# Kernel optimization log

Measured on AMD Instinct MI355X. Metric: run time of the kernel, lower is better.

Reference implementation:

```python
import jax, jax.numpy as jnp
import numpy as np

B, T, D, P, ALPHA, PR = 4, 4096, 1024, 512, 4, 64


def setup_inputs() -> dict:
    key = jax.random.key(0)
    ks = jax.random.split(key, 9)
    g = lambda k, shape, scale: jax.random.normal(k, shape, jnp.float32) * scale
    return {
        "x": jax.random.normal(ks[0], (B, T, D), jnp.float32),
        "W_toP": g(ks[1], (D, P), D ** -0.5),
        "W_U": g(ks[2], (D, P, ALPHA), D ** -0.5),
        "W_F": g(ks[3], (D, P), D ** -0.5),
        "W_V": g(ks[4], (P, ALPHA), 1.0),
        "W_lam": g(ks[5], (P, PR), P ** -0.5),
        "B_mat": g(ks[6], (P, PR), P ** -0.5),
        "C_mat": g(ks[7], (PR, P), PR ** -0.5),
        "W_fromP": g(ks[8], (P, D), P ** -0.5),
    }


def reference(x, W_toP, W_U, W_F, W_V, W_lam, B_mat, C_mat, W_fromP):
    # dense pre-path: (B,T,D)->(B,T,P)
    pre = jnp.einsum('btd,dp->btp', x, W_toP)
    # CeptaEmbedding dense pathway: multi-factor projection U, gates F, weighted Y
    U = jnp.einsum('btd,dpa->btpa', x, W_U)            # (B,T,P,alpha)
    Fg = jax.nn.sigmoid(jnp.einsum('btd,dp->btp', x, W_F))  # (B,T,P) in (0,1)
    Y = U * W_V                                        # (B,T,P,alpha)
    # CeptaRouting(reduce='sum'): sum over alpha factors, plus residual pre-path
    t = Y.sum(-1) + pre                                # (B,T,P)
    # CeptaSSMLowRank: input-dependent diagonal decay in rank-PR state space
    lam = jax.nn.sigmoid(jnp.einsum('btp,pr->btr', Fg, W_lam))  # (B,T,PR)
    u_in = jnp.einsum('btp,pr->btr', t, B_mat)                  # (B,T,PR)

    def step(s, inp):
        l, u = inp
        s = l * s + u
        return s, s

    s0 = jnp.zeros((x.shape[0], PR), x.dtype)
    _, s_seq = jax.lax.scan(step, s0, (lam.transpose(1, 0, 2), u_in.transpose(1, 0, 2)))
    s_seq = s_seq.transpose(1, 0, 2)                   # (B,T,PR)
    t_tilde = t + jnp.einsum('btr,rp->btp', s_seq, C_mat)
    h = jnp.einsum('btp,pd->btd', t_tilde, W_fromP)    # dropout p=0 -> identity
    return h
```

## Files before the change

kernel.cpp:

```cpp
#include <hip/hip_runtime.h>
#include <hip/hip_bf16.h>

#define Bb 4
#define Tt 4096
#define Dd 1024
#define Pp 512
#define PRr 64
#define Mm (Bb*Tt)
#define NCH 64
#define CL  64

typedef __bf16 bf16;
typedef __bf16 bf16x8 __attribute__((ext_vector_type(8)));
typedef __bf16 bf16x4 __attribute__((ext_vector_type(4)));
typedef float f32x4 __attribute__((ext_vector_type(4)));

#define GPTR(p) (const __attribute__((address_space(1))) void*)(p)
#define LPTR(p) (__attribute__((address_space(3))) void*)(p)

__device__ __forceinline__ float sigmoidf_(float x) {
    return 1.0f / (1.0f + __expf(-x));
}


__global__ void prep_w1(const float* __restrict__ W_toP, const float* __restrict__ W_U,
                        const float* __restrict__ W_V, const float* __restrict__ W_F,
                        bf16* __restrict__ W1t) {
    int idx = blockIdx.x * 256 + threadIdx.x;
    int n = idx >> 10, k = idx & 1023;
    float v;
    if (n < Pp) {
        int p = n;
        float4 u  = *(const float4*)(W_U + ((size_t)k * Pp + p) * 4);
        float4 wv = *(const float4*)(W_V + (size_t)p * 4);
        v = W_toP[(size_t)k * Pp + p] + u.x * wv.x + u.y * wv.y + u.z * wv.z + u.w * wv.w;
    } else {
        v = W_F[(size_t)k * Pp + (n - Pp)];
    }
    W1t[idx] = (bf16)v;
}

__global__ void prep_w3(const float* __restrict__ B_mat, const float* __restrict__ W_lam,
                        bf16* __restrict__ W3t) {
    int idx = blockIdx.x * 256 + threadIdx.x;
    int n = idx >> 10, k = idx & 1023;
    float v = 0.0f;
    if (n < PRr) { if (k < Pp) v = B_mat[(size_t)k * PRr + n]; }
    else         { if (k >= Pp) v = W_lam[(size_t)(k - Pp) * PRr + (n - PRr)]; }
    W3t[idx] = (bf16)v;
}

__global__ void prep_w2(const float* __restrict__ W_fromP, const float* __restrict__ C_mat,
                        bf16* __restrict__ W2t) {
    int n = blockIdx.x;
    int k = threadIdx.x;
    float v;
    if (k < Pp) {
        v = W_fromP[(size_t)k * Dd + n];
    } else {
        int r = k - Pp;
        float acc = 0.0f;
        #pragma unroll 8
        for (int p = 0; p < Pp; p++)
            acc = fmaf(C_mat[(size_t)r * Pp + p], W_fromP[(size_t)p * Dd + n], acc);
        v = acc;
    }
    W2t[(size_t)n * 576 + k] = (bf16)v;
}

__global__ void cast_x(const float* __restrict__ x, bf16* __restrict__ xb) {
    int i = blockIdx.x * 256 + threadIdx.x;
    float4 v = ((const float4*)x)[i];
    bf16x4 o;
    o[0] = (bf16)v.x; o[1] = (bf16)v.y; o[2] = (bf16)v.z; o[3] = (bf16)v.w;
    ((bf16x4*)xb)[i] = o;
}

__global__ void scan_phase1(const float* __restrict__ UL,
                            float* __restrict__ slocal, float* __restrict__ pprod,
                            float* __restrict__ carryS, float* __restrict__ carryP) {
    int b = blockIdx.y, c = blockIdx.x, r = threadIdx.x;
    const float* ulb = UL + ((size_t)b * Tt + (size_t)c * CL) * 128;
    float* sl = slocal + ((size_t)b * Tt + (size_t)c * CL) * PRr;
    float* pp = pprod  + ((size_t)b * Tt + (size_t)c * CL) * PRr;
    float s = 0.0f, p = 1.0f;
    for (int t0 = 0; t0 < CL; t0 += 16) {
        float uv[16], lv[16];
        #pragma unroll
        for (int i = 0; i < 16; i++) {
            uv[i] = ulb[(size_t)(t0 + i) * 128 + r];
            lv[i] = ulb[(size_t)(t0 + i) * 128 + 64 + r];
        }
        #pragma unroll
        for (int i = 0; i < 16; i++) {
            s = fmaf(lv[i], s, uv[i]);
            p *= lv[i];
            sl[(size_t)(t0 + i) * PRr + r] = s;
            pp[(size_t)(t0 + i) * PRr + r] = p;
        }
    }
    int ci = b * NCH + c;
    carryS[(size_t)ci * PRr + r] = s;
    carryP[(size_t)ci * PRr + r] = p;
}

__global__ void scan_phase2(const float* __restrict__ carryS, const float* __restrict__ carryP,
                            float* __restrict__ carryIn) {
    int b = blockIdx.x, r = threadIdx.x;
    float carry = 0.0f;
    for (int c0 = 0; c0 < NCH; c0 += 16) {
        float cs[16], cp[16];
        #pragma unroll
        for (int i = 0; i < 16; i++) {
            size_t idx = ((size_t)b * NCH + c0 + i) * PRr + r;
            cs[i] = carryS[idx];
            cp[i] = carryP[idx];
        }
        #pragma unroll
        for (int i = 0; i < 16; i++) {
            carryIn[((size_t)b * NCH + c0 + i) * PRr + r] = carry;
            carry = fmaf(cp[i], carry, cs[i]);
        }
    }
}

__global__ void scan_phase3(const float* __restrict__ slocal, const float* __restrict__ pprod,
                            const float* __restrict__ carryIn, bf16* __restrict__ sb) {
    int i = blockIdx.x * 256 + threadIdx.x;
    int r = i & (PRr - 1);
    int row = i >> 6;
    int b = row >> 12;
    int t = row & (Tt - 1);
    int c = t / CL;
    float carry = carryIn[((size_t)b * NCH + c) * PRr + r];
    sb[i] = (bf16)fmaf(pprod[i], carry, slocal[i]);
}

template <int EPI>
__global__ __launch_bounds__(512, 2) void gemm256(
    const bf16* __restrict__ A0, int lda0,
    const bf16* __restrict__ A1, int lda1, int ksplit,
    const bf16* __restrict__ Bt, int ldb, int K,
    void* __restrict__ Cout, int ldc, int sigcol) {

    __shared__ bf16 As[2][256 * 64];
    __shared__ bf16 Bs[2][256 * 64];

    const int tid  = threadIdx.x;
    const int lane = tid & 63;
    const int wid  = tid >> 6;
    const int wm   = wid >> 2;
    const int wn   = wid & 3;

    const int cpx = gridDim.x >> 3;
    const int bid = blockIdx.x;
    const int swz = (bid & 7) * cpx + (bid >> 3);
    const int mBase = (swz >> 2) * 256;
    const int nBase = (swz & 3) * 256;

    const int lr  = lane & 15;
    const int q16 = (lane >> 4) * 16;

    auto srcA = [&](int kt, const bf16*& src, int& lda, int& kc) {
        if (kt < ksplit) { src = A0; lda = lda0; kc = kt; }
        else             { src = A1; lda = lda1; kc = kt - ksplit; }
    };

    auto stage = [&](const bf16* src, int lda, int kc, int rowBase, bf16* lbuf, int rd) {
        int d = rd * 8192 + tid * 16;
        int L = d ^ (((d >> 7) & 7) << 4);
        int r = L >> 7;
        int c = (L & 127) >> 1;
        const bf16* g = src + (size_t)(rowBase + r) * lda + (kc + c);
        __builtin_amdgcn_global_load_lds(GPTR(g), LPTR((char*)lbuf + d), 16, 0, 0);
    };

    auto frag = [&](const bf16* lbuf, int r, int cb) -> bf16x8 {
        int flat = r * 128 + cb;
        int phys = flat ^ (((flat >> 7) & 7) << 4);
        return *(const bf16x8*)((const char*)lbuf + phys);
    };

    const int NT = K / 64;

    {
        const bf16* sa; int la, kc; srcA(0, sa, la, kc);
        stage(sa, la, kc, mBase, As[0], 0); stage(sa, la, kc, mBase, As[0], 1);
        stage(sa, la, kc, mBase, As[0], 2); stage(sa, la, kc, mBase, As[0], 3);
        stage(Bt, ldb, 0, nBase, Bs[0], 0); stage(Bt, ldb, 0, nBase, Bs[0], 1);
        stage(Bt, ldb, 0, nBase, Bs[0], 2); stage(Bt, ldb, 0, nBase, Bs[0], 3);
    }
    asm volatile("s_waitcnt vmcnt(0)" ::: "memory");
    __builtin_amdgcn_s_barrier();

    f32x4 acc[8][4] = {};
    bf16x8 aX[4], aY[4], b0[4], b1[4];

    #pragma unroll
    for (int i = 0; i < 4; ++i) aX[i] = frag(As[0], wm * 128 + i * 16 + lr, q16);
    #pragma unroll
    for (int i = 0; i < 4; ++i) b0[i] = frag(Bs[0], wn * 64 + i * 16 + lr, q16);

    for (int t = 0; t < NT; ++t) {
        bf16* Ac = As[t & 1];       bf16* Bc = Bs[t & 1];
        bf16* An = As[(t + 1) & 1]; bf16* Bn = Bs[(t + 1) & 1];
        const bool hn = (t + 1 < NT);

        if (hn) {
            const bf16* sa; int la, kc; srcA((t + 1) * 64, sa, la, kc);
            const int ktn = (t + 1) * 64;
            stage(sa, la, kc, mBase, An, 0); stage(sa, la, kc, mBase, An, 1);
            stage(sa, la, kc, mBase, An, 2); stage(sa, la, kc, mBase, An, 3);
            stage(Bt, ldb, ktn, nBase, Bn, 0); stage(Bt, ldb, ktn, nBase, Bn, 1);
            stage(Bt, ldb, ktn, nBase, Bn, 2); stage(Bt, ldb, ktn, nBase, Bn, 3);
        }

        #pragma unroll
        for (int i = 0; i < 4; ++i) aY[i] = frag(Ac, wm * 128 + (i + 4) * 16 + lr, q16);
        __builtin_amdgcn_s_setprio(1);
        #pragma unroll
        for (int m = 0; m < 4; ++m)
            #pragma unroll
            for (int n = 0; n < 4; ++n)
                acc[m][n] = __builtin_amdgcn_mfma_f32_16x16x32_bf16(aX[m], b0[n], acc[m][n], 0, 0, 0);
        __builtin_amdgcn_s_setprio(0);

        #pragma unroll
        for (int i = 0; i < 4; ++i) aX[i] = frag(Ac, wm * 128 + i * 16 + lr, 64 + q16);
        #pragma unroll
        for (int i = 0; i < 4; ++i) b1[i] = frag(Bc, wn * 64 + i * 16 + lr, 64 + q16);
        __builtin_amdgcn_s_setprio(1);
        #pragma unroll
        for (int m = 0; m < 4; ++m)
            #pragma unroll
            for (int n = 0; n < 4; ++n)
                acc[m + 4][n] = __builtin_amdgcn_mfma_f32_16x16x32_bf16(aY[m], b0[n], acc[m + 4][n], 0, 0, 0);
        __builtin_amdgcn_s_setprio(0);

        #pragma unroll
        for (int i = 0; i < 4; ++i) aY[i] = frag(Ac, wm * 128 + (i + 4) * 16 + lr, 64 + q16);
        __builtin_amdgcn_s_setprio(1);
        #pragma unroll
        for (int m = 0; m < 4; ++m)
            #pragma unroll
            for (int n = 0; n < 4; ++n)
                acc[m][n] = __builtin_amdgcn_mfma_f32_16x16x32_bf16(aX[m], b1[n], acc[m][n], 0, 0, 0);
        __builtin_amdgcn_s_setprio(0);

        __builtin_amdgcn_s_setprio(1);
        #pragma unroll
        for (int m = 0; m < 4; ++m)
            #pragma unroll
            for (int n = 0; n < 4; ++n)
                acc[m + 4][n] = __builtin_amdgcn_mfma_f32_16x16x32_bf16(aY[m], b1[n], acc[m + 4][n], 0, 0, 0);
        __builtin_amdgcn_s_setprio(0);

        if (hn) {
            asm volatile("s_waitcnt vmcnt(0)" ::: "memory");
            __builtin_amdgcn_s_barrier();
            #pragma unroll
            for (int i = 0; i < 4; ++i) aX[i] = frag(An, wm * 128 + i * 16 + lr, q16);
            #pragma unroll
            for (int i = 0; i < 4; ++i) b0[i] = frag(Bn, wn * 64 + i * 16 + lr, q16);
        }
    }

    const int lr4 = (lane >> 4) * 4;
    #pragma unroll
    for (int m = 0; m < 8; ++m) {
        #pragma unroll
        for (int n = 0; n < 4; ++n) {
            #pragma unroll
            for (int j = 0; j < 4; ++j) {
                int row = mBase + wm * 128 + m * 16 + lr4 + j;
                int col = nBase + wn * 64 + n * 16 + lr;
                float v = acc[m][n][j];
                if (EPI == 0) {
                    if (col >= sigcol) v = sigmoidf_(v);
                    ((bf16*)Cout)[(size_t)row * ldc + col] = (bf16)v;
                } else {
                    ((float*)Cout)[(size_t)row * ldc + col] = v;
                }
            }
        }
    }
}

template <int EPI>
__global__ __launch_bounds__(256) void gemm_bt(
    const bf16* __restrict__ A0, int lda0,
    const bf16* __restrict__ A1, int lda1, int ksplit,
    const bf16* __restrict__ Bt, int K,
    void* __restrict__ Cout, int ldc, int sigcol) {

    __shared__ bf16 As[128][32];
    __shared__ bf16 Bs[128][32];

    const int tid  = threadIdx.x;
    const int lane = tid & 63;
    const int wid  = tid >> 6;
    const int wr   = (wid >> 1) * 64;
    const int wc   = (wid & 1) * 64;
    const int mBase = blockIdx.x * 128;
    const int nBase = blockIdx.y * 128;

    f32x4 acc[4][4] = {};

    const int lr = lane & 15;
    const int lk = (lane >> 4) * 8;

    for (int kt = 0; kt < K; kt += 32) {
        const bf16* Asrc; int lda_; int kcol;
        if (kt < ksplit) { Asrc = A0; lda_ = lda0; kcol = kt; }
        else             { Asrc = A1; lda_ = lda1; kcol = kt - ksplit; }

        __syncthreads();
        #pragma unroll
        for (int i = 0; i < 2; i++) {
            int c = tid + i * 256;
            int row = c >> 2, k8 = (c & 3) * 8;
            const bf16* g = Asrc + (size_t)(mBase + row) * lda_ + (kcol + k8);
            __builtin_amdgcn_global_load_lds(GPTR(g), LPTR(&As[0][0] + c * 8), 16, 0, 0);
        }
        #pragma unroll
        for (int i = 0; i < 2; i++) {
            int c = tid + i * 256;
            int row = c >> 2, k8 = (c & 3) * 8;
            const bf16* g = Bt + (size_t)(nBase + row) * K + (kt + k8);
            __builtin_amdgcn_global_load_lds(GPTR(g), LPTR(&Bs[0][0] + c * 8), 16, 0, 0);
        }
        __syncthreads();

        bf16x8 af[4], bfr[4];
        #pragma unroll
        for (int m = 0; m < 4; m++) af[m]  = *(const bf16x8*)(&As[wr + m * 16 + lr][lk]);
        #pragma unroll
        for (int n = 0; n < 4; n++) bfr[n] = *(const bf16x8*)(&Bs[wc + n * 16 + lr][lk]);
        #pragma unroll
        for (int m = 0; m < 4; m++)
            #pragma unroll
            for (int n = 0; n < 4; n++)
                acc[m][n] = __builtin_amdgcn_mfma_f32_16x16x32_bf16(af[m], bfr[n], acc[m][n], 0, 0, 0);
    }

    const int lr4 = (lane >> 4) * 4;
    const int lc  = lane & 15;
    #pragma unroll
    for (int m = 0; m < 4; m++) {
        #pragma unroll
        for (int n = 0; n < 4; n++) {
            #pragma unroll
            for (int j = 0; j < 4; j++) {
                int row = mBase + wr + m * 16 + lr4 + j;
                int col = nBase + wc + n * 16 + lc;
                float v = acc[m][n][j];
                if (EPI == 1) {
                    if (col >= sigcol) v = sigmoidf_(v);
                    ((float*)Cout)[(size_t)row * ldc + col] = v;
                } else {
                    ((float*)Cout)[(size_t)row * ldc + col] = v;
                }
            }
        }
    }
}

extern "C" void kernel_launch(void* const* d_in, const int* in_sizes, int n_in,
                              void* d_out, int out_size, void* d_ws, size_t ws_size,
                              hipStream_t stream) {
    const float* x       = (const float*)d_in[0];
    const float* W_toP   = (const float*)d_in[1];
    const float* W_U     = (const float*)d_in[2];
    const float* W_F     = (const float*)d_in[3];
    const float* W_V     = (const float*)d_in[4];
    const float* W_lam   = (const float*)d_in[5];
    const float* B_mat   = (const float*)d_in[6];
    const float* C_mat   = (const float*)d_in[7];
    const float* W_fromP = (const float*)d_in[8];
    float* out = (float*)d_out;

    char* ws = (char*)d_ws;
    size_t off = 0;
    auto alloc = [&](size_t bytes) { void* p = ws + off; off = (off + bytes + 255) & ~255ULL; return p; };
    bf16*  xb  = (bf16*)alloc((size_t)Mm * Dd * 2);
    bf16*  TF  = (bf16*)alloc((size_t)Mm * 1024 * 2);
    float* UL  = (float*)alloc((size_t)Mm * 128 * 4);
    bf16*  sb  = (bf16*)alloc((size_t)Mm * PRr * 2);
    bf16*  W1t = (bf16*)alloc((size_t)1024 * 1024 * 2);
    bf16*  W3t = (bf16*)alloc((size_t)128 * 1024 * 2);
    bf16*  W2t = (bf16*)alloc((size_t)1024 * 576 * 2);
    float* slocal = (float*)alloc((size_t)Mm * PRr * 4);
    float* pprod  = (float*)alloc((size_t)Mm * PRr * 4);
    float* carryS = (float*)alloc((size_t)Bb * NCH * PRr * 4);
    float* carryP = (float*)alloc((size_t)Bb * NCH * PRr * 4);
    float* carryI = (float*)alloc((size_t)Bb * NCH * PRr * 4);

    prep_w1<<<dim3(4096), dim3(256), 0, stream>>>(W_toP, W_U, W_V, W_F, W1t);
    prep_w3<<<dim3(512),  dim3(256), 0, stream>>>(B_mat, W_lam, W3t);
    prep_w2<<<dim3(1024), dim3(576), 0, stream>>>(W_fromP, C_mat, W2t);
    cast_x <<<dim3(Mm * Dd / 4 / 256), dim3(256), 0, stream>>>(x, xb);

    gemm256<0><<<dim3((Mm / 256) * (1024 / 256)), 512, 0, stream>>>(
        xb, Dd, xb, Dd, 1 << 30, W1t, Dd, Dd, TF, 1024, Pp);

    gemm_bt<1><<<dim3(Mm / 128, 1), 256, 0, stream>>>(
        TF, 1024, TF, 1024, 1 << 30, W3t, 1024, UL, 128, PRr);

    scan_phase1<<<dim3(NCH, Bb), dim3(PRr), 0, stream>>>(UL, slocal, pprod, carryS, carryP);
    scan_phase2<<<dim3(Bb), dim3(PRr), 0, stream>>>(carryS, carryP, carryI);
    scan_phase3<<<dim3(Mm * PRr / 256), dim3(256), 0, stream>>>(slocal, pprod, carryI, sb);

    gemm256<2><<<dim3((Mm / 256) * (1024 / 256)), 512, 0, stream>>>(
        TF, 1024, sb, PRr, Pp, W2t, 576, 576, out, Dd, 1 << 30);
}
```

Measured before the change: 163.2 us.

## Interleave split global-to-LDS staging with MFMA phases using partial vmcnt waits

Restructures the GEMM main loop so the next tile's global_load_lds stages are spread across the four MFMA sub-phases instead of being issued all at once. Each stage is followed by a partial vmcnt wait and extra barriers, so that loads for the current tile can finish while compute proceeds. The prologue is reordered the same way. The aim is to smooth memory traffic and lower register pressure by using a single A-fragment buffer. In exchange it adds many more barriers per iteration and depends on subtle vmcnt ordering for correctness.

```diff
diff --git a/kernel.cpp b/kernel.cpp
--- a/kernel.cpp
+++ b/kernel.cpp
@@ -185,84 +185,88 @@
 
     {
         const bf16* sa; int la, kc; srcA(0, sa, la, kc);
-        stage(sa, la, kc, mBase, As[0], 0); stage(sa, la, kc, mBase, As[0], 1);
-        stage(sa, la, kc, mBase, As[0], 2); stage(sa, la, kc, mBase, As[0], 3);
+        stage(sa, la, kc, mBase, As[0], 0); stage(sa, la, kc, mBase, As[0], 2);
         stage(Bt, ldb, 0, nBase, Bs[0], 0); stage(Bt, ldb, 0, nBase, Bs[0], 1);
         stage(Bt, ldb, 0, nBase, Bs[0], 2); stage(Bt, ldb, 0, nBase, Bs[0], 3);
-    }
-    asm volatile("s_waitcnt vmcnt(0)" ::: "memory");
+        stage(sa, la, kc, mBase, As[0], 1); stage(sa, la, kc, mBase, As[0], 3);
+    }
+    asm volatile("s_waitcnt vmcnt(2)" ::: "memory");
     __builtin_amdgcn_s_barrier();
 
     f32x4 acc[8][4] = {};
-    bf16x8 aX[4], aY[4], b0[4], b1[4];
-
-    #pragma unroll
-    for (int i = 0; i < 4; ++i) aX[i] = frag(As[0], wm * 128 + i * 16 + lr, q16);
-    #pragma unroll
-    for (int i = 0; i < 4; ++i) b0[i] = frag(Bs[0], wn * 64 + i * 16 + lr, q16);
+    bf16x8 a[4], b0[4], b1[4];
 
     for (int t = 0; t < NT; ++t) {
         bf16* Ac = As[t & 1];       bf16* Bc = Bs[t & 1];
         bf16* An = As[(t + 1) & 1]; bf16* Bn = Bs[(t + 1) & 1];
         const bool hn = (t + 1 < NT);
-
+        const bf16* sa = A0; int la = lda0, kc = 0;
+        if (hn) srcA((t + 1) * 64, sa, la, kc);
+        const int ktn = (t + 1) * 64;
+
+        #pragma unroll
+        for (int i = 0; i < 4; ++i) a[i]  = frag(Ac, wm * 128 + i * 16 + lr, q16);
+        #pragma unroll
+        for (int i = 0; i < 4; ++i) b0[i] = frag(Bc, wn * 64 + i * 16 + lr, q16);
         if (hn) {
-            const bf16* sa; int la, kc; srcA((t + 1) * 64, sa, la, kc);
-            const int ktn = (t + 1) * 64;
-            stage(sa, la, kc, mBase, An, 0); stage(sa, la, kc, mBase, An, 1);
-            stage(sa, la, kc, mBase, An, 2); stage(sa, la, kc, mBase, An, 3);
-            stage(Bt, ldb, ktn, nBase, Bn, 0); stage(Bt, ldb, ktn, nBase, Bn, 1);
-            stage(Bt, ldb, ktn, nBase, Bn, 2); stage(Bt, ldb, ktn, nBase, Bn, 3);
-        }
-
-        #pragma unroll
-        for (int i = 0; i < 4; ++i) aY[i] = frag(Ac, wm * 128 + (i + 4) * 16 + lr, q16);
+            stage(sa, la, kc, mBase, An, 0); stage(sa, la, kc, mBase, An, 2);
+            asm volatile("s_waitcnt vmcnt(2)" ::: "memory");
+        } else {
+            asm volatile("s_waitcnt vmcnt(0)" ::: "memory");
+        }
+        __builtin_amdgcn_s_barrier();
         __builtin_amdgcn_s_setprio(1);
         #pragma unroll
         for (int m = 0; m < 4; ++m)
             #pragma unroll
             for (int n = 0; n < 4; ++n)
-                acc[m][n] = __builtin_amdgcn_mfma_f32_16x16x32_bf16(aX[m], b0[n], acc[m][n], 0, 0, 0);
+                acc[m][n] = __builtin_amdgcn_mfma_f32_16x16x32_bf16(a[m], b0[n], acc[m][n], 0, 0, 0);
         __builtin_amdgcn_s_setprio(0);
-
-        #pragma unroll
-        for (int i = 0; i < 4; ++i) aX[i] = frag(Ac, wm * 128 + i * 16 + lr, 64 + q16);
+        __builtin_amdgcn_s_barrier();
+
+        #pragma unroll
+        for (int i = 0; i < 4; ++i) a[i] = frag(Ac, wm * 128 + (i + 4) * 16 + lr, q16);
+        if (hn) { stage(Bt, ldb, ktn, nBase, Bn, 0); stage(Bt, ldb, ktn, nBase, Bn, 1); }
+        __builtin_amdgcn_s_barrier();
+        __builtin_amdgcn_s_setprio(1);
+        #pragma unroll
+        for (int m = 0; m < 4; ++m)
+            #pragma unroll
+            for (int n = 0; n < 4; ++n)
+                acc[m + 4][n] = __builtin_amdgcn_mfma_f32_16x16x32_bf16(a[m], b0[n], acc[m + 4][n], 0, 0, 0);
+        __builtin_amdgcn_s_setprio(0);
+        __builtin_amdgcn_s_barrier();
+
+        #pragma unroll
+        for (int i = 0; i < 4; ++i) a[i]  = frag(Ac, wm * 128 + i * 16 + lr, 64 + q16);
         #pragma unroll
         for (int i = 0; i < 4; ++i) b1[i] = frag(Bc, wn * 64 + i * 16 + lr, 64 + q16);
+        if (hn) { stage(Bt, ldb, ktn, nBase, Bn, 2); stage(Bt, ldb, ktn, nBase, Bn, 3); }
+        __builtin_amdgcn_s_barrier();
         __builtin_amdgcn_s_setprio(1);
         #pragma unroll
         for (int m = 0; m < 4; ++m)
             #pragma unroll
             for (int n = 0; n < 4; ++n)
-                acc[m + 4][n] = __builtin_amdgcn_mfma_f32_16x16x32_bf16(aY[m], b0[n], acc[m + 4][n], 0, 0, 0);
+                acc[m][n] = __builtin_amdgcn_mfma_f32_16x16x32_bf16(a[m], b1[n], acc[m][n], 0, 0, 0);
         __builtin_amdgcn_s_setprio(0);
-
-        #pragma unroll
-        for (int i = 0; i < 4; ++i) aY[i] = frag(Ac, wm * 128 + (i + 4) * 16 + lr, 64 + q16);
+        __builtin_amdgcn_s_barrier();
+
+        #pragma unroll
+        for (int i = 0; i < 4; ++i) a[i] = frag(Ac, wm * 128 + (i + 4) * 16 + lr, 64 + q16);
+        if (hn) {
+            stage(sa, la, kc, mBase, An, 1); stage(sa, la, kc, mBase, An, 3);
+            asm volatile("s_waitcnt vmcnt(2)" ::: "memory");
+        }
+        __builtin_amdgcn_s_barrier();
         __builtin_amdgcn_s_setprio(1);
         #pragma unroll
         for (int m = 0; m < 4; ++m)
             #pragma unroll
             for (int n = 0; n < 4; ++n)
-                acc[m][n] = __builtin_amdgcn_mfma_f32_16x16x32_bf16(aX[m], b1[n], acc[m][n], 0, 0, 0);
+                acc[m + 4][n] = __builtin_amdgcn_mfma_f32_16x16x32_bf16(a[m], b1[n], acc[m + 4][n], 0, 0, 0);
         __builtin_amdgcn_s_setprio(0);
-
-        __builtin_amdgcn_s_setprio(1);
-        #pragma unroll
-        for (int m = 0; m < 4; ++m)
-            #pragma unroll
-            for (int n = 0; n < 4; ++n)
-                acc[m + 4][n] = __builtin_amdgcn_mfma_f32_16x16x32_bf16(aY[m], b1[n], acc[m + 4][n], 0, 0, 0);
-        __builtin_amdgcn_s_setprio(0);
-
-        if (hn) {
-            asm volatile("s_waitcnt vmcnt(0)" ::: "memory");
-            __builtin_amdgcn_s_barrier();
-            #pragma unroll
-            for (int i = 0; i < 4; ++i) aX[i] = frag(An, wm * 128 + i * 16 + lr, q16);
-            #pragma unroll
-            for (int i = 0; i < 4; ++i) b0[i] = frag(Bn, wn * 64 + i * 16 + lr, q16);
-        }
+        __builtin_amdgcn_s_barrier();
     }
 
     const int lr4 = (lane >> 4) * 4;
```

New measurement: 160.7 us. Within noise of the previous version (-1.5%).
